# Kernel tuning notes

Measured on AMD Instinct MI355X. Metric: run time of the kernel, lower is better.

Reference implementation:

```python
import jax, jax.numpy as jnp
import numpy as np

T = 4096       # batch of observations
REPR = 2048    # repr_dim
FEAT = 1024    # feature_dim
HID = 1024     # hidden_dim (MoE input/output dim)
GATE = 256     # moe_gate_dim
MH = 256       # moe_hidden_dim (per-expert hidden)
E = 32         # num_experts
K = 4          # top_k
ACT = 12       # action dim
EPS = 1e-5


def setup_inputs() -> dict:
    key = jax.random.key(0)
    ks = jax.random.split(key, 18)

    def lin(k, fan_in, shape):
        return jax.random.normal(k, shape, jnp.float32) * (1.0 / np.sqrt(fan_in))

    return {
        "obs": jax.random.normal(ks[0], (T, REPR), jnp.float32),
        "std": jnp.ones((1,), jnp.float32),
        "trunk_w": lin(ks[1], REPR, (REPR, FEAT)),
        "trunk_b": jnp.zeros((FEAT,), jnp.float32),
        "ln_g": jnp.ones((FEAT,), jnp.float32),
        "ln_b": jnp.zeros((FEAT,), jnp.float32),
        "p1_w": lin(ks[2], FEAT, (FEAT, HID)),
        "p1_b": jnp.zeros((HID,), jnp.float32),
        "g1_w": lin(ks[3], HID, (HID, GATE)),
        "g1_b": jnp.zeros((GATE,), jnp.float32),
        "g2_w": lin(ks[4], GATE, (GATE, E)),
        "g2_b": jnp.zeros((E,), jnp.float32),
        "ew1": lin(ks[5], HID, (E, HID, MH)),
        "eb1": jnp.zeros((E, MH), jnp.float32),
        "ew2": lin(ks[6], MH, (E, MH, HID)),
        "eb2": jnp.zeros((E, HID), jnp.float32),
        "p2_w": lin(ks[7], HID, (HID, ACT)),
        "p2_b": jnp.zeros((ACT,), jnp.float32),
    }


def layer_norm(x, g, b):
    m = jnp.mean(x, -1, keepdims=True)
    v = jnp.var(x, -1, keepdims=True)
    return (x - m) * jax.lax.rsqrt(v + EPS) * g + b


def moe(x, g1_w, g1_b, g2_w, g2_b, ew1, eb1, ew2, eb2):
    # gate MLP: [T, HID] -> [T, E]
    logits = jax.nn.relu(x @ g1_w + g1_b) @ g2_w + g2_b
    probs = jax.nn.softmax(logits, axis=-1)                 # [T, E]
    topv, topi = jax.lax.top_k(probs, K)                    # [T, K]
    w = topv / jnp.sum(topv, -1, keepdims=True)             # renormalized top-k weights
    n = x.shape[0]
    combine = jnp.zeros((n, E), x.dtype).at[jnp.arange(n)[:, None], topi].set(w)  # [T, E]
    # per-expert 2-layer MLP (dense dispatch, masked combine)
    h = jax.nn.relu(jnp.einsum('td,edh->teh', x, ew1) + eb1)   # [T, E, MH]
    y = jnp.einsum('teh,eho->teo', h, ew2) + eb2               # [T, E, HID]
    out = jnp.einsum('te,teo->to', combine, y)                 # [T, HID]
    # load-balancing aux loss (switch-style)
    importance = jnp.mean(probs, axis=0)                                  # [E]
    load = jnp.sum(jax.nn.one_hot(topi, E, dtype=x.dtype), (0, 1)) / (n * K)
    aux = E * jnp.sum(importance * load)
    return out, aux


def reference(obs, std, trunk_w, trunk_b, ln_g, ln_b, p1_w, p1_b,
              g1_w, g1_b, g2_w, g2_b, ew1, eb1, ew2, eb2, p2_w, p2_b):
    h = jnp.tanh(layer_norm(obs @ trunk_w + trunk_b, ln_g, ln_b))
    x = jax.nn.relu(h @ p1_w + p1_b)
    x, aux = moe(x, g1_w, g1_b, g2_w, g2_b, ew1, eb1, ew2, eb2)
    mu = jnp.tanh(jax.nn.relu(x) @ p2_w + p2_b)
    std_out = jnp.ones_like(mu) * std
    return mu, std_out, aux
```

## Files before the change

kernel.cpp:

```cpp
#include <hip/hip_runtime.h>
#include <math.h>

#define T_DIM  4096
#define REPR_D 2048
#define FEAT_D 1024
#define HID_D  1024
#define GATE_D 256
#define MH_D   256
#define NE     32
#define TOPK   4
#define ACT_D  12
#define LN_EPS 1e-5f
#define NB_G   (T_DIM / 8)

typedef unsigned short u16;
typedef __attribute__((ext_vector_type(8))) _Float16 f16x8;
typedef __attribute__((ext_vector_type(4))) float f32x4;
typedef __attribute__((ext_vector_type(4))) unsigned short u16x4;

__device__ __forceinline__ u16 f2h_bits(float f) {
  _Float16 h = (_Float16)f;
  return __builtin_bit_cast(u16, h);
}
__device__ __forceinline__ float h2f(u16 v) {
  return (float)__builtin_bit_cast(_Float16, v);
}
__device__ __forceinline__ void split2h(float v, u16* h0, u16* h1) {
  _Float16 a = (_Float16)v;
  float r = v - (float)a;
  *h0 = __builtin_bit_cast(u16, a);
  *h1 = f2h_bits(r * 2048.0f);
}

__device__ __forceinline__ void gload16(const u16* g, u16* l) {
  __builtin_amdgcn_global_load_lds(
      (const __attribute__((address_space(1))) unsigned int*)g,
      (__attribute__((address_space(3))) unsigned int*)l, 16, 0, 0);
}

__global__ __launch_bounds__(256)
void gemm_f16x2_sk(const u16* __restrict__ A, const u16* __restrict__ Bt,
                   float* __restrict__ Cp, int M, int N, int K) {
  __shared__ u16 lA[2][128 * 64];
  __shared__ u16 lB[2][64 * 64];
  const int tid = threadIdx.x;
  const unsigned gx = gridDim.x, gy = gridDim.y;
  const unsigned lin = blockIdx.x + gx * (blockIdx.y + gy * blockIdx.z);
  const unsigned q = (gx * gy * gridDim.z) >> 3;
  const unsigned swz = (lin & 7) * q + (lin >> 3);
  const int bn = (swz % gx) * 64;
  const int bm = ((swz / gx) % gy) * 128;
  const int bz = swz / (gx * gy);
  const int ksl = K / gridDim.z;
  const int kbeg = bz * ksl, kend = kbeg + ksl;
  const int lane = tid & 63, wid = tid >> 6;
  const int wm = (wid >> 1) * 64, wn = (wid & 1) * 32;
  const size_t sA = (size_t)M * K, sB = (size_t)N * K;
  const int srow = tid >> 3;
  const int coff = ((tid & 7) ^ (srow & 7)) * 8;
  const u16* pa = A + (size_t)(bm + srow) * K + coff;
  const u16* pb = Bt + (size_t)(bn + srow) * K + coff;
  u16* la = &lA[0][0] + tid * 8;
  u16* lb = &lB[0][0] + tid * 8;
  const int fr = lane & 15, sx = lane >> 4, rx = lane & 7;
  f32x4 acc1[4][2] = {}, acc2[4][2] = {};
  for (int k0 = kbeg; k0 < kend; k0 += 64) {
    #pragma unroll
    for (int p = 0; p < 2; ++p) {
      #pragma unroll
      for (int s = 0; s < 4; ++s)
        gload16(pa + p * sA + (size_t)(s * 32) * K + k0, la + p * 8192 + s * 2048);
      #pragma unroll
      for (int s = 0; s < 2; ++s)
        gload16(pb + p * sB + (size_t)(s * 32) * K + k0, lb + p * 4096 + s * 2048);
    }
    __syncthreads();
    #pragma unroll
    for (int kh = 0; kh < 2; ++kh) {
      const int sa = (((kh << 2) | sx) ^ rx) * 8;
      f16x8 af0[4], af1[4], bq[2];
      #pragma unroll
      for (int m = 0; m < 4; ++m) {
        af0[m] = *(const f16x8*)&lA[0][(wm + m * 16 + fr) * 64 + sa];
        af1[m] = *(const f16x8*)&lA[1][(wm + m * 16 + fr) * 64 + sa];
      }
      #pragma unroll
      for (int n = 0; n < 2; ++n)
        bq[n] = *(const f16x8*)&lB[0][(wn + n * 16 + fr) * 64 + sa];
      #pragma unroll
      for (int m = 0; m < 4; ++m)
        #pragma unroll
        for (int n = 0; n < 2; ++n) {
          acc1[m][n] = __builtin_amdgcn_mfma_f32_16x16x32_f16(af0[m], bq[n], acc1[m][n], 0, 0, 0);
          acc2[m][n] = __builtin_amdgcn_mfma_f32_16x16x32_f16(af1[m], bq[n], acc2[m][n], 0, 0, 0);
        }
      #pragma unroll
      for (int n = 0; n < 2; ++n)
        bq[n] = *(const f16x8*)&lB[1][(wn + n * 16 + fr) * 64 + sa];
      #pragma unroll
      for (int m = 0; m < 4; ++m)
        #pragma unroll
        for (int n = 0; n < 2; ++n)
          acc2[m][n] = __builtin_amdgcn_mfma_f32_16x16x32_f16(af0[m], bq[n], acc2[m][n], 0, 0, 0);
    }
    __syncthreads();
  }
  float* Co = Cp + (size_t)bz * M * N;
  #pragma unroll
  for (int n = 0; n < 2; ++n) {
    const int col = bn + wn + n * 16 + (lane & 15);
    #pragma unroll
    for (int m = 0; m < 4; ++m) {
      #pragma unroll
      for (int r = 0; r < 4; ++r) {
        const int row = bm + wm + m * 16 + (lane >> 4) * 4 + r;
        Co[(size_t)row * N + col] = acc1[m][n][r] + acc2[m][n][r] * (1.0f / 2048.0f);
      }
    }
  }
}

__global__ __launch_bounds__(256)
void expert_l1(const u16* __restrict__ x, const u16* __restrict__ ew1T,
               const float* __restrict__ eb1, const int* __restrict__ perm,
               const int* __restrict__ offsets, const int* __restrict__ counts,
               u16* __restrict__ hbuf) {
  const int e = blockIdx.z;
  const int cnt = counts[e];
  const int r0 = blockIdx.y * 128;
  if (r0 >= cnt) return;
  const int base = offsets[e];
  const int bn = blockIdx.x * 64;
  __shared__ u16 lA[128 * 64];
  __shared__ u16 lB[64 * 64];
  __shared__ int toksm[128];
  const int tid = threadIdx.x;
  if (tid < 128) toksm[tid] = (r0 + tid < cnt) ? (perm[base + r0 + tid] >> 2) : 0;
  __syncthreads();
  const int lane = tid & 63, wid = tid >> 6;
  const int wm = (wid >> 1) * 64, wn = (wid & 1) * 32;
  const int srow = tid >> 3;
  const int coff = ((tid & 7) ^ (srow & 7)) * 8;
  const u16* pa[4]; const u16* pb[2];
  #pragma unroll
  for (int s = 0; s < 4; ++s)
    pa[s] = x + (size_t)toksm[srow + 32 * s] * HID_D + coff;
  #pragma unroll
  for (int s = 0; s < 2; ++s)
    pb[s] = ew1T + (size_t)e * MH_D * HID_D + (size_t)(bn + srow + 32 * s) * HID_D + coff;
  u16* la = lA + tid * 8;
  u16* lb = lB + tid * 8;
  const int fr = lane & 15, sx = lane >> 4, rx = lane & 7;
  f32x4 acc[4][2] = {};
  for (int k0 = 0; k0 < HID_D; k0 += 64) {
    #pragma unroll
    for (int s = 0; s < 4; ++s) gload16(pa[s] + k0, la + s * 2048);
    #pragma unroll
    for (int s = 0; s < 2; ++s) gload16(pb[s] + k0, lb + s * 2048);
    __syncthreads();
    #pragma unroll
    for (int kh = 0; kh < 2; ++kh) {
      const int sa = (((kh << 2) | sx) ^ rx) * 8;
      f16x8 af[4], bq[2];
      #pragma unroll
      for (int m = 0; m < 4; ++m)
        af[m] = *(const f16x8*)&lA[(wm + m * 16 + fr) * 64 + sa];
      #pragma unroll
      for (int n = 0; n < 2; ++n)
        bq[n] = *(const f16x8*)&lB[(wn + n * 16 + fr) * 64 + sa];
      #pragma unroll
      for (int m = 0; m < 4; ++m)
        #pragma unroll
        for (int n = 0; n < 2; ++n)
          acc[m][n] = __builtin_amdgcn_mfma_f32_16x16x32_f16(af[m], bq[n], acc[m][n], 0, 0, 0);
    }
    __syncthreads();
  }
  #pragma unroll
  for (int n = 0; n < 2; ++n) {
    const int col = bn + wn + n * 16 + (lane & 15);
    const float bz = eb1[e * MH_D + col];
    #pragma unroll
    for (int m = 0; m < 4; ++m) {
      #pragma unroll
      for (int r = 0; r < 4; ++r) {
        const int rl = wm + m * 16 + (lane >> 4) * 4 + r;
        if (r0 + rl < cnt) {
          const float v = fmaxf(acc[m][n][r] + bz, 0.f);
          hbuf[(size_t)(base + r0 + rl) * MH_D + col] = f2h_bits(v);
        }
      }
    }
  }
}

__global__ __launch_bounds__(256)
void expert_l2(const u16* __restrict__ hbuf, const u16* __restrict__ ew2T,
               const float* __restrict__ eb2, const int* __restrict__ offsets,
               const int* __restrict__ counts, u16* __restrict__ ybuf) {
  const int e = blockIdx.z;
  const int cnt = counts[e];
  const int r0 = blockIdx.y * 128;
  if (r0 >= cnt) return;
  const int base = offsets[e];
  const int bn = blockIdx.x * 64;
  __shared__ u16 lA[128 * 64];
  __shared__ u16 lB[64 * 64];
  const int tid = threadIdx.x;
  const int lane = tid & 63, wid = tid >> 6;
  const int wm = (wid >> 1) * 64, wn = (wid & 1) * 32;
  const int srow = tid >> 3;
  const int coff = ((tid & 7) ^ (srow & 7)) * 8;
  const u16* pa[4]; const u16* pb[2];
  #pragma unroll
  for (int s = 0; s < 4; ++s) {
    const int rr = r0 + srow + 32 * s;
    const int rc = (rr < cnt) ? rr : cnt - 1;
    pa[s] = hbuf + (size_t)(base + rc) * MH_D + coff;
  }
  #pragma unroll
  for (int s = 0; s < 2; ++s)
    pb[s] = ew2T + (size_t)e * HID_D * MH_D + (size_t)(bn + srow + 32 * s) * MH_D + coff;
  u16* la = lA + tid * 8;
  u16* lb = lB + tid * 8;
  const int fr = lane & 15, sx = lane >> 4, rx = lane & 7;
  f32x4 acc[4][2] = {};
  for (int k0 = 0; k0 < MH_D; k0 += 64) {
    #pragma unroll
    for (int s = 0; s < 4; ++s) gload16(pa[s] + k0, la + s * 2048);
    #pragma unroll
    for (int s = 0; s < 2; ++s) gload16(pb[s] + k0, lb + s * 2048);
    __syncthreads();
    #pragma unroll
    for (int kh = 0; kh < 2; ++kh) {
      const int sa = (((kh << 2) | sx) ^ rx) * 8;
      f16x8 af[4], bq[2];
      #pragma unroll
      for (int m = 0; m < 4; ++m)
        af[m] = *(const f16x8*)&lA[(wm + m * 16 + fr) * 64 + sa];
      #pragma unroll
      for (int n = 0; n < 2; ++n)
        bq[n] = *(const f16x8*)&lB[(wn + n * 16 + fr) * 64 + sa];
      #pragma unroll
      for (int m = 0; m < 4; ++m)
        #pragma unroll
        for (int n = 0; n < 2; ++n)
          acc[m][n] = __builtin_amdgcn_mfma_f32_16x16x32_f16(af[m], bq[n], acc[m][n], 0, 0, 0);
    }
    __syncthreads();
  }
  #pragma unroll
  for (int n = 0; n < 2; ++n) {
    const int col = bn + wn + n * 16 + (lane & 15);
    const float bz = eb2[e * HID_D + col];
    #pragma unroll
    for (int m = 0; m < 4; ++m) {
      #pragma unroll
      for (int r = 0; r < 4; ++r) {
        const int rl = wm + m * 16 + (lane >> 4) * 4 + r;
        if (r0 + rl < cnt)
          ybuf[(size_t)(base + r0 + rl) * HID_D + col] = f2h_bits(acc[m][n][r] + bz);
      }
    }
  }
}

__global__ __launch_bounds__(256)
void cast2h_k(const float* __restrict__ in, u16* __restrict__ out, size_t total) {
  const size_t i = ((size_t)blockIdx.x * 256 + threadIdx.x) * 4;
  const float4 v = *(const float4*)(in + i);
  const float vv[4] = {v.x, v.y, v.z, v.w};
  u16x4 o0, o1;
  #pragma unroll
  for (int j = 0; j < 4; ++j) {
    u16 a, b;
    split2h(vv[j], &a, &b);
    o0[j] = a; o1[j] = b;
  }
  *(u16x4*)(out + i) = o0;
  *(u16x4*)(out + total + i) = o1;
}

__global__ __launch_bounds__(256)
void transpose_cast2h(const float* __restrict__ in, u16* __restrict__ out, int K, int N) {
  __shared__ float t[32][33];
  const int bn = blockIdx.x * 32, bk = blockIdx.y * 32;
  const int tx = threadIdx.x & 31, ty = threadIdx.x >> 5;
  const size_t NK = (size_t)N * K;
  #pragma unroll
  for (int i = 0; i < 32; i += 8) t[ty + i][tx] = in[(size_t)(bk + ty + i) * N + bn + tx];
  __syncthreads();
  #pragma unroll
  for (int i = 0; i < 32; i += 8) {
    const size_t idx = (size_t)(bn + ty + i) * K + bk + tx;
    u16 h0, h1;
    split2h(t[tx][ty + i], &h0, &h1);
    out[idx] = h0; out[idx + NK] = h1;
  }
}

__global__ __launch_bounds__(256)
void transpose_casth(const float* __restrict__ in, u16* __restrict__ out, int K, int N) {
  const size_t off = (size_t)blockIdx.z * K * N;
  in += off; out += off;
  __shared__ float t[32][33];
  const int bn = blockIdx.x * 32, bk = blockIdx.y * 32;
  const int tx = threadIdx.x & 31, ty = threadIdx.x >> 5;
  #pragma unroll
  for (int i = 0; i < 32; i += 8) t[ty + i][tx] = in[(size_t)(bk + ty + i) * N + bn + tx];
  __syncthreads();
  #pragma unroll
  for (int i = 0; i < 32; i += 8) out[(size_t)(bn + ty + i) * K + bk + tx] = f2h_bits(t[tx][ty + i]);
}

__global__ __launch_bounds__(256)
void ln_tanh2h(const float* __restrict__ hp, const float* __restrict__ tb,
               u16* __restrict__ outp, const float* __restrict__ g,
               const float* __restrict__ b) {
  const int row = blockIdx.x, tid = threadIdx.x;
  const size_t MN = (size_t)T_DIM * FEAT_D;
  const float4 va = ((const float4*)(hp + (size_t)row * FEAT_D))[tid];
  const float4 vb = ((const float4*)(hp + MN + (size_t)row * FEAT_D))[tid];
  const float4 vt = ((const float4*)tb)[tid];
  float4 v;
  v.x = va.x + vb.x + vt.x; v.y = va.y + vb.y + vt.y;
  v.z = va.z + vb.z + vt.z; v.w = va.w + vb.w + vt.w;
  float s = v.x + v.y + v.z + v.w;
  float ss = v.x * v.x + v.y * v.y + v.z * v.z + v.w * v.w;
  #pragma unroll
  for (int d = 32; d >= 1; d >>= 1) { s += __shfl_xor(s, d, 64); ss += __shfl_xor(ss, d, 64); }
  __shared__ float red[2][4];
  const int w = tid >> 6;
  if ((tid & 63) == 0) { red[0][w] = s; red[1][w] = ss; }
  __syncthreads();
  s  = red[0][0] + red[0][1] + red[0][2] + red[0][3];
  ss = red[1][0] + red[1][1] + red[1][2] + red[1][3];
  const float m = s * (1.f / FEAT_D);
  const float inv = rsqrtf(ss * (1.f / FEAT_D) - m * m + LN_EPS);
  const float4 gg = ((const float4*)g)[tid];
  const float4 bb = ((const float4*)b)[tid];
  const float tv[4] = {tanhf((v.x - m) * inv * gg.x + bb.x),
                       tanhf((v.y - m) * inv * gg.y + bb.y),
                       tanhf((v.z - m) * inv * gg.z + bb.z),
                       tanhf((v.w - m) * inv * gg.w + bb.w)};
  u16x4 o0, o1;
  #pragma unroll
  for (int j = 0; j < 4; ++j) {
    u16 a, c;
    split2h(tv[j], &a, &c);
    o0[j] = a; o1[j] = c;
  }
  ((u16x4*)(outp + (size_t)row * FEAT_D))[tid] = o0;
  ((u16x4*)(outp + MN + (size_t)row * FEAT_D))[tid] = o1;
}

__global__ __launch_bounds__(256)
void combine2_relu_split2h(const float* __restrict__ P, const float* __restrict__ bias,
                           u16* __restrict__ out2) {
  const size_t MN = (size_t)T_DIM * HID_D;
  const size_t i = ((size_t)blockIdx.x * 256 + threadIdx.x) * 4;
  const float4 a = *(const float4*)(P + i);
  const float4 b = *(const float4*)(P + MN + i);
  const float4 bz = *(const float4*)(bias + (i & (HID_D - 1)));
  const float vv[4] = {fmaxf(a.x + b.x + bz.x, 0.f), fmaxf(a.y + b.y + bz.y, 0.f),
                       fmaxf(a.z + b.z + bz.z, 0.f), fmaxf(a.w + b.w + bz.w, 0.f)};
  u16x4 o0, o1;
  #pragma unroll
  for (int j = 0; j < 4; ++j) {
    u16 h0, h1;
    split2h(vv[j], &h0, &h1);
    o0[j] = h0; o1[j] = h1;
  }
  *(u16x4*)(out2 + i) = o0;
  *(u16x4*)(out2 + MN + i) = o1;
}

__global__ __launch_bounds__(256)
void gate2_topk(const float* __restrict__ hgP, const float* __restrict__ g1b,
                const float* __restrict__ g2w, const float* __restrict__ g2b,
                float* __restrict__ blkimp, int* __restrict__ blkcnt,
                int* __restrict__ topi, float* __restrict__ topw,
                int* __restrict__ lrank) {
  __shared__ float wsm[GATE_D][NE];
  __shared__ float rows[8][GATE_D];
  __shared__ float pacc[8][NE];
  __shared__ int lhist[NE];
  const int tid = threadIdx.x;
  const int t0 = blockIdx.x * 8;
  const size_t TG = (size_t)T_DIM * GATE_D;
  if (tid < NE) lhist[tid] = 0;
  {
    float4* wv = (float4*)&wsm[0][0];
    const float4* gv = (const float4*)g2w;
    #pragma unroll
    for (int i = 0; i < 8; ++i) wv[tid + 256 * i] = gv[tid + 256 * i];
  }
  {
    const float4* p0 = (const float4*)hgP;
    const float4* p1 = (const float4*)(hgP + TG);
    const float4* p2 = (const float4*)(hgP + 2 * TG);
    const float4* p3 = (const float4*)(hgP + 3 * TG);
    const float4* bv = (const float4*)g1b;
    float4* rv = (float4*)&rows[0][0];
    #pragma unroll
    for (int i = 0; i < 2; ++i) {
      const int idx = tid + 256 * i;
      const int r = idx >> 6, c4 = idx & 63;
      const size_t gidx = (size_t)(t0 + r) * (GATE_D / 4) + c4;
      const float4 a = p0[gidx], b = p1[gidx], c = p2[gidx], d = p3[gidx];
      const float4 bb = bv[c4];
      float4 v;
      v.x = fmaxf(a.x + b.x + c.x + d.x + bb.x, 0.f);
      v.y = fmaxf(a.y + b.y + c.y + d.y + bb.y, 0.f);
      v.z = fmaxf(a.z + b.z + c.z + d.z + bb.z, 0.f);
      v.w = fmaxf(a.w + b.w + c.w + d.w + bb.w, 0.f);
      rv[idx] = v;
    }
  }
  __syncthreads();
  const int tl = tid >> 5;
  const int e  = tid & 31;
  const int t  = t0 + tl;
  float a8[8] = {};
  #pragma unroll
  for (int k0 = 0; k0 < GATE_D; k0 += 8)
    #pragma unroll
    for (int j = 0; j < 8; ++j)
      a8[j] = fmaf(rows[tl][k0 + j], wsm[k0 + j][e], a8[j]);
  const float logit = g2b[e] +
      (((a8[0] + a8[1]) + (a8[2] + a8[3])) + ((a8[4] + a8[5]) + (a8[6] + a8[7])));
  float m = logit;
  #pragma unroll
  for (int d = 16; d >= 1; d >>= 1) m = fmaxf(m, __shfl_xor(m, d, 32));
  const float p = expf(logit - m);
  float ssum = p;
  #pragma unroll
  for (int d = 16; d >= 1; d >>= 1) ssum += __shfl_xor(ssum, d, 32);
  const float prob = p / ssum;
  pacc[tl][e] = prob;
  __syncthreads();
  if (tl == 0) {
    float a = 0.f;
    #pragma unroll
    for (int q = 0; q < 8; ++q) a += pacc[q][e];
    blkimp[blockIdx.x * NE + e] = a;
  }
  float cur = prob;
  float wv[TOPK]; int wi[TOPK];
  #pragma unroll
  for (int it = 0; it < TOPK; ++it) {
    float v = cur; int idx = e;
    #pragma unroll
    for (int d = 16; d >= 1; d >>= 1) {
      float v2 = __shfl_xor(v, d, 32);
      int   i2 = __shfl_xor(idx, d, 32);
      if (v2 > v || (v2 == v && i2 < idx)) { v = v2; idx = i2; }
    }
    wv[it] = v; wi[it] = idx;
    if (e == idx) cur = -1e30f;
  }
  if (e == 0) {
    const float s4 = wv[0] + wv[1] + wv[2] + wv[3];
    #pragma unroll
    for (int k2 = 0; k2 < TOPK; ++k2) {
      topi[t * TOPK + k2] = wi[k2];
      topw[t * TOPK + k2] = wv[k2] / s4;
      lrank[t * TOPK + k2] = atomicAdd(&lhist[wi[k2]], 1);
    }
  }
  __syncthreads();
  if (tid < NE) blkcnt[blockIdx.x * NE + tid] = lhist[tid];
}

__global__ __launch_bounds__(256)
void scan_k(const int* __restrict__ blkcnt, int* __restrict__ counts,
            int* __restrict__ offsets, int* __restrict__ blkbase) {
  __shared__ int segsum[8][NE];
  __shared__ int soff[8][NE];
  const int e = threadIdx.x & 31, seg = threadIdx.x >> 5;
  const int b0 = seg * 64;
  int vals[64];
  #pragma unroll
  for (int i = 0; i < 64; ++i) vals[i] = blkcnt[(b0 + i) * NE + e];
  int run = 0;
  #pragma unroll
  for (int i = 0; i < 64; ++i) { const int c = vals[i]; vals[i] = run; run += c; }
  segsum[seg][e] = run;
  __syncthreads();
  if (seg == 0) {
    int acc = 0;
    #pragma unroll
    for (int s2 = 0; s2 < 8; ++s2) { soff[s2][e] = acc; acc += segsum[s2][e]; }
    counts[e] = acc;
  }
  __syncthreads();
  if (threadIdx.x == 0) {
    int a = 0;
    for (int i = 0; i < NE; ++i) { offsets[i] = a; a += counts[i]; }
    offsets[NE] = a;
  }
  const int sb = soff[seg][e];
  #pragma unroll
  for (int i = 0; i < 64; ++i) blkbase[(b0 + i) * NE + e] = sb + vals[i];
}

__global__ __launch_bounds__(256)
void fill_perm2(const int* __restrict__ topi, const int* __restrict__ lrank,
                const int* __restrict__ blkbase, const int* __restrict__ offsets,
                int* __restrict__ perm, int* __restrict__ inv) {
  const int s = blockIdx.x * 256 + threadIdx.x;
  const int e = topi[s];
  const int b = s >> 5;
  const int pos = offsets[e] + blkbase[b * NE + e] + lrank[s];
  perm[pos] = s;
  inv[s] = pos;
}

__global__ __launch_bounds__(256)
void p2_head(const u16* __restrict__ ybuf, const int* __restrict__ inv,
             const float* __restrict__ topw, const float* __restrict__ w,
             const float* __restrict__ b, const float* __restrict__ stdp,
             float* __restrict__ outp) {
  const int t = (blockIdx.x * 256 + threadIdx.x) >> 6;
  const int lane = threadIdx.x & 63;
  if (t >= T_DIM) return;
  const int p0 = inv[t * 4 + 0], p1 = inv[t * 4 + 1];
  const int p2 = inv[t * 4 + 2], p3 = inv[t * 4 + 3];
  const float w0 = topw[t * 4 + 0], w1 = topw[t * 4 + 1];
  const float w2 = topw[t * 4 + 2], w3 = topw[t * 4 + 3];
  const u16* y0 = ybuf + (size_t)p0 * HID_D;
  const u16* y1 = ybuf + (size_t)p1 * HID_D;
  const u16* y2 = ybuf + (size_t)p2 * HID_D;
  const u16* y3 = ybuf + (size_t)p3 * HID_D;
  float a[ACT_D] = {};
  for (int k = lane; k < HID_D; k += 64) {
    float xv = w0 * h2f(y0[k]) + w1 * h2f(y1[k]) + w2 * h2f(y2[k]) + w3 * h2f(y3[k]);
    xv = fmaxf(xv, 0.f);
    const float* wr = w + (size_t)k * ACT_D;
    #pragma unroll
    for (int j = 0; j < ACT_D; ++j) a[j] = fmaf(xv, wr[j], a[j]);
  }
  #pragma unroll
  for (int j = 0; j < ACT_D; ++j) {
    float v = a[j];
    #pragma unroll
    for (int d = 32; d >= 1; d >>= 1) v += __shfl_xor(v, d, 64);
    a[j] = v;
  }
  if (lane == 0) {
    const float sv = stdp[0];
    #pragma unroll
    for (int j = 0; j < ACT_D; ++j) {
      outp[(size_t)t * ACT_D + j] = tanhf(a[j] + b[j]);
      outp[(size_t)T_DIM * ACT_D + (size_t)t * ACT_D + j] = sv;
    }
  }
}

__global__ __launch_bounds__(256)
void aux_kernel(const float* __restrict__ blkimp, const int* __restrict__ counts,
                float* __restrict__ outp) {
  __shared__ float part[8][NE];
  const int e = threadIdx.x & 31, seg = threadIdx.x >> 5;
  float a = 0.f;
  #pragma unroll
  for (int i = 0; i < 64; ++i) a += blkimp[((seg << 6) + i) * NE + e];
  part[seg][e] = a;
  __syncthreads();
  if (threadIdx.x < 32) {
    float impe = 0.f;
    #pragma unroll
    for (int s2 = 0; s2 < 8; ++s2) impe += part[s2][e];
    float v = (impe / (float)T_DIM) * ((float)counts[e] / (float)(T_DIM * TOPK));
    #pragma unroll
    for (int d = 16; d >= 1; d >>= 1) v += __shfl_xor(v, d, 32);
    if (e == 0) outp[2 * T_DIM * ACT_D] = (float)NE * v;
  }
}

extern "C" void kernel_launch(void* const* d_in, const int* in_sizes, int n_in,
                              void* d_out, int out_size, void* d_ws, size_t ws_size,
                              hipStream_t stream) {
  const float* obs     = (const float*)d_in[0];
  const float* stdp    = (const float*)d_in[1];
  const float* trunk_w = (const float*)d_in[2];
  const float* trunk_b = (const float*)d_in[3];
  const float* ln_g    = (const float*)d_in[4];
  const float* ln_b    = (const float*)d_in[5];
  const float* p1_w    = (const float*)d_in[6];
  const float* p1_b    = (const float*)d_in[7];
  const float* g1_w    = (const float*)d_in[8];
  const float* g1_b    = (const float*)d_in[9];
  const float* g2_w    = (const float*)d_in[10];
  const float* g2_b    = (const float*)d_in[11];
  const float* ew1     = (const float*)d_in[12];
  const float* eb1     = (const float*)d_in[13];
  const float* ew2     = (const float*)d_in[14];
  const float* eb2     = (const float*)d_in[15];
  const float* p2_w    = (const float*)d_in[16];
  const float* p2_b    = (const float*)d_in[17];
  float* out = (float*)d_out;

  char* p = (char*)d_ws;
  u16*   obs2 = (u16*)p;
  u16*   h2   = (u16*)p;
  float* hgP  = (float*)p;
  u16*   x2   = (u16*)(p + 2 * (size_t)T_DIM * FEAT_D * 2);
  p += 2 * (size_t)T_DIM * REPR_D * 2;
  u16* trunk_wT2 = (u16*)p;
  u16* p1_wT2    = (u16*)p;
  u16* g1_wT2    = (u16*)(p + 2 * (size_t)FEAT_D * HID_D * 2);
  u16* hbuf      = (u16*)p;
  p += 2 * (size_t)REPR_D * FEAT_D * 2;
  float* hpP  = (float*)p;
  float* p1P  = (float*)p;
  u16*   ybuf = (u16*)p;
  p += 2 * (size_t)T_DIM * FEAT_D * 4;
  u16* ew1T = (u16*)p; p += (size_t)NE * HID_D * MH_D * 2;
  u16* ew2T = (u16*)p; p += (size_t)NE * HID_D * MH_D * 2;
  float* topw    = (float*)p; p += (size_t)T_DIM * TOPK * 4;
  int*   topi    = (int*)p;   p += (size_t)T_DIM * TOPK * 4;
  int*   perm    = (int*)p;   p += (size_t)T_DIM * TOPK * 4;
  int*   inv     = (int*)p;   p += (size_t)T_DIM * TOPK * 4;
  int*   lrank   = (int*)p;   p += (size_t)T_DIM * TOPK * 4;
  float* blkimp  = (float*)p; p += (size_t)NB_G * NE * 4;
  int*   blkcnt  = (int*)p;   p += (size_t)NB_G * NE * 4;
  int*   blkbase = (int*)p;   p += (size_t)NB_G * NE * 4;
  int*   counts  = (int*)p;   p += 128;
  int*   offsets = (int*)p;   p += 256;

  cast2h_k<<<(T_DIM * REPR_D) / 1024, 256, 0, stream>>>(obs, obs2, (size_t)T_DIM * REPR_D);
  transpose_cast2h<<<dim3(FEAT_D / 32, REPR_D / 32), 256, 0, stream>>>(trunk_w, trunk_wT2, REPR_D, FEAT_D);

  gemm_f16x2_sk<<<dim3(FEAT_D / 64, T_DIM / 128, 2), 256, 0, stream>>>(
      obs2, trunk_wT2, hpP, T_DIM, FEAT_D, REPR_D);
  transpose_cast2h<<<dim3(HID_D / 32, FEAT_D / 32), 256, 0, stream>>>(p1_w, p1_wT2, FEAT_D, HID_D);
  transpose_cast2h<<<dim3(GATE_D / 32, HID_D / 32), 256, 0, stream>>>(g1_w, g1_wT2, HID_D, GATE_D);

  ln_tanh2h<<<T_DIM, 256, 0, stream>>>(hpP, trunk_b, h2, ln_g, ln_b);

  gemm_f16x2_sk<<<dim3(HID_D / 64, T_DIM / 128, 2), 256, 0, stream>>>(
      h2, p1_wT2, p1P, T_DIM, HID_D, FEAT_D);
  combine2_relu_split2h<<<(T_DIM * HID_D) / 1024, 256, 0, stream>>>(p1P, p1_b, x2);

  gemm_f16x2_sk<<<dim3(GATE_D / 64, T_DIM / 128, 4), 256, 0, stream>>>(
      x2, g1_wT2, hgP, T_DIM, GATE_D, HID_D);

  gate2_topk<<<NB_G, 256, 0, stream>>>(hgP, g1_b, g2_w, g2_b, blkimp, blkcnt, topi, topw, lrank);
  scan_k<<<1, 256, 0, stream>>>(blkcnt, counts, offsets, blkbase);
  fill_perm2<<<(T_DIM * TOPK) / 256, 256, 0, stream>>>(topi, lrank, blkbase, offsets, perm, inv);

  transpose_casth<<<dim3(MH_D / 32, HID_D / 32, NE), 256, 0, stream>>>(ew1, ew1T, HID_D, MH_D);
  transpose_casth<<<dim3(HID_D / 32, MH_D / 32, NE), 256, 0, stream>>>(ew2, ew2T, MH_D, HID_D);
  expert_l1<<<dim3(MH_D / 64, 32, NE), 256, 0, stream>>>(
      x2, ew1T, eb1, perm, offsets, counts, hbuf);
  expert_l2<<<dim3(HID_D / 64, 32, NE), 256, 0, stream>>>(
      hbuf, ew2T, eb2, offsets, counts, ybuf);

  p2_head<<<T_DIM / 4, 256, 0, stream>>>(ybuf, inv, topw, p2_w, p2_b, stdp, out);
  aux_kernel<<<1, 256, 0, stream>>>(blkimp, counts, out);
}
```

Before: 268.4 us.

## Double-buffer LDS in GEMM and expert kernels with 32-wide K stages; vectorize head loads

The split-K GEMM and both expert MLP kernels now stage K in 32-element slices into two LDS buffers. The next slice's global-to-LDS load is issued while MFMAs run on the current one, which takes one barrier per stage off the critical load path, and the XOR swizzle is reworked to match the narrower rows. The p2 head also reads expert outputs with 4-wide vector loads instead of scalar half loads. The trade is more barriers overall from halving the K step, and less latency hiding if the loads do not complete behind the compute.

New measurement: 298.1 us. +11.1%, slower.

```diff
diff --git a/kernel.cpp b/kernel.cpp
--- a/kernel.cpp
+++ b/kernel.cpp
@@ -41,8 +41,8 @@
 __global__ __launch_bounds__(256)
 void gemm_f16x2_sk(const u16* __restrict__ A, const u16* __restrict__ Bt,
                    float* __restrict__ Cp, int M, int N, int K) {
-  __shared__ u16 lA[2][128 * 64];
-  __shared__ u16 lB[2][64 * 64];
+  __shared__ u16 lA[2 * 2 * 128 * 32];
+  __shared__ u16 lB[2 * 2 * 64 * 32];
   const int tid = threadIdx.x;
   const unsigned gx = gridDim.x, gy = gridDim.y;
   const unsigned lin = blockIdx.x + gx * (blockIdx.y + gy * blockIdx.z);
@@ -52,57 +52,65 @@
   const int bm = ((swz / gx) % gy) * 128;
   const int bz = swz / (gx * gy);
   const int ksl = K / gridDim.z;
-  const int kbeg = bz * ksl, kend = kbeg + ksl;
+  const int kbeg = bz * ksl;
+  const int nst = ksl / 32;
   const int lane = tid & 63, wid = tid >> 6;
   const int wm = (wid >> 1) * 64, wn = (wid & 1) * 32;
   const size_t sA = (size_t)M * K, sB = (size_t)N * K;
-  const int srow = tid >> 3;
-  const int coff = ((tid & 7) ^ (srow & 7)) * 8;
-  const u16* pa = A + (size_t)(bm + srow) * K + coff;
-  const u16* pb = Bt + (size_t)(bn + srow) * K + coff;
-  u16* la = &lA[0][0] + tid * 8;
-  u16* lb = &lB[0][0] + tid * 8;
-  const int fr = lane & 15, sx = lane >> 4, rx = lane & 7;
+  const u16* pa[4]; const u16* pb[2];
+  #pragma unroll
+  for (int s = 0; s < 4; ++s) {
+    const int c = tid + 256 * s;
+    const int pl = c >> 9, r = (c >> 2) & 127, sl = c & 3;
+    pa[s] = A + (size_t)pl * sA + (size_t)(bm + r) * K + kbeg + ((sl ^ ((r >> 1) & 3)) << 3);
+  }
+  #pragma unroll
+  for (int s = 0; s < 2; ++s) {
+    const int c = tid + 256 * s;
+    const int pl = c >> 8, r = (c >> 2) & 63, sl = c & 3;
+    pb[s] = Bt + (size_t)pl * sB + (size_t)(bn + r) * K + kbeg + ((sl ^ ((r >> 1) & 3)) << 3);
+  }
+  const int fr = lane & 15, sx = lane >> 4;
   f32x4 acc1[4][2] = {}, acc2[4][2] = {};
-  for (int k0 = kbeg; k0 < kend; k0 += 64) {
-    #pragma unroll
-    for (int p = 0; p < 2; ++p) {
-      #pragma unroll
-      for (int s = 0; s < 4; ++s)
-        gload16(pa + p * sA + (size_t)(s * 32) * K + k0, la + p * 8192 + s * 2048);
-      #pragma unroll
-      for (int s = 0; s < 2; ++s)
-        gload16(pb + p * sB + (size_t)(s * 32) * K + k0, lb + p * 4096 + s * 2048);
-    }
-    __syncthreads();
-    #pragma unroll
-    for (int kh = 0; kh < 2; ++kh) {
-      const int sa = (((kh << 2) | sx) ^ rx) * 8;
-      f16x8 af0[4], af1[4], bq[2];
-      #pragma unroll
-      for (int m = 0; m < 4; ++m) {
-        af0[m] = *(const f16x8*)&lA[0][(wm + m * 16 + fr) * 64 + sa];
-        af1[m] = *(const f16x8*)&lA[1][(wm + m * 16 + fr) * 64 + sa];
+  #pragma unroll
+  for (int s = 0; s < 4; ++s) gload16(pa[s], lA + (tid + 256 * s) * 8);
+  #pragma unroll
+  for (int s = 0; s < 2; ++s) gload16(pb[s], lB + (tid + 256 * s) * 8);
+  __syncthreads();
+  for (int t = 0; t < nst; ++t) {
+    const int cur = t & 1, nxt = cur ^ 1;
+    if (t + 1 < nst) {
+      const int kk = (t + 1) * 32;
+      #pragma unroll
+      for (int s = 0; s < 4; ++s) gload16(pa[s] + kk, lA + nxt * 8192 + (tid + 256 * s) * 8);
+      #pragma unroll
+      for (int s = 0; s < 2; ++s) gload16(pb[s] + kk, lB + nxt * 4096 + (tid + 256 * s) * 8);
+    }
+    const u16* bufA = lA + cur * 8192;
+    const u16* bufB = lB + cur * 4096;
+    f16x8 af0[4], af1[4], bq0[2], bq1[2];
+    #pragma unroll
+    for (int m = 0; m < 4; ++m) {
+      const int row = wm + m * 16 + fr;
+      const int so = (sx ^ ((row >> 1) & 3)) << 3;
+      af0[m] = *(const f16x8*)&bufA[row * 32 + so];
+      af1[m] = *(const f16x8*)&bufA[4096 + row * 32 + so];
+    }
+    #pragma unroll
+    for (int n = 0; n < 2; ++n) {
+      const int row = wn + n * 16 + fr;
+      const int so = (sx ^ ((row >> 1) & 3)) << 3;
+      bq0[n] = *(const f16x8*)&bufB[row * 32 + so];
+      bq1[n] = *(const f16x8*)&bufB[2048 + row * 32 + so];
+    }
+    #pragma unroll
+    for (int m = 0; m < 4; ++m)
+      #pragma unroll
+      for (int n = 0; n < 2; ++n) {
+        acc1[m][n] = __builtin_amdgcn_mfma_f32_16x16x32_f16(af0[m], bq0[n], acc1[m][n], 0, 0, 0);
+        acc2[m][n] = __builtin_amdgcn_mfma_f32_16x16x32_f16(af1[m], bq0[n], acc2[m][n], 0, 0, 0);
+        acc2[m][n] = __builtin_amdgcn_mfma_f32_16x16x32_f16(af0[m], bq1[n], acc2[m][n], 0, 0, 0);
       }
-      #pragma unroll
-      for (int n = 0; n < 2; ++n)
-        bq[n] = *(const f16x8*)&lB[0][(wn + n * 16 + fr) * 64 + sa];
-      #pragma unroll
-      for (int m = 0; m < 4; ++m)
-        #pragma unroll
-        for (int n = 0; n < 2; ++n) {
-          acc1[m][n] = __builtin_amdgcn_mfma_f32_16x16x32_f16(af0[m], bq[n], acc1[m][n], 0, 0, 0);
-          acc2[m][n] = __builtin_amdgcn_mfma_f32_16x16x32_f16(af1[m], bq[n], acc2[m][n], 0, 0, 0);
-        }
-      #pragma unroll
-      for (int n = 0; n < 2; ++n)
-        bq[n] = *(const f16x8*)&lB[1][(wn + n * 16 + fr) * 64 + sa];
-      #pragma unroll
-      for (int m = 0; m < 4; ++m)
-        #pragma unroll
-        for (int n = 0; n < 2; ++n)
-          acc2[m][n] = __builtin_amdgcn_mfma_f32_16x16x32_f16(af0[m], bq[n], acc2[m][n], 0, 0, 0);
-    }
     __syncthreads();
   }
   float* Co = Cp + (size_t)bz * M * N;
@@ -131,49 +139,58 @@
   if (r0 >= cnt) return;
   const int base = offsets[e];
   const int bn = blockIdx.x * 64;
-  __shared__ u16 lA[128 * 64];
-  __shared__ u16 lB[64 * 64];
+  __shared__ u16 lA[2 * 128 * 32];
+  __shared__ u16 lB[2 * 64 * 32];
   __shared__ int toksm[128];
   const int tid = threadIdx.x;
   if (tid < 128) toksm[tid] = (r0 + tid < cnt) ? (perm[base + r0 + tid] >> 2) : 0;
   __syncthreads();
   const int lane = tid & 63, wid = tid >> 6;
   const int wm = (wid >> 1) * 64, wn = (wid & 1) * 32;
-  const int srow = tid >> 3;
-  const int coff = ((tid & 7) ^ (srow & 7)) * 8;
-  const u16* pa[4]; const u16* pb[2];
-  #pragma unroll
-  for (int s = 0; s < 4; ++s)
-    pa[s] = x + (size_t)toksm[srow + 32 * s] * HID_D + coff;
-  #pragma unroll
-  for (int s = 0; s < 2; ++s)
-    pb[s] = ew1T + (size_t)e * MH_D * HID_D + (size_t)(bn + srow + 32 * s) * HID_D + coff;
-  u16* la = lA + tid * 8;
-  u16* lb = lB + tid * 8;
-  const int fr = lane & 15, sx = lane >> 4, rx = lane & 7;
+  const u16* pa[2]; const u16* pb;
+  #pragma unroll
+  for (int s = 0; s < 2; ++s) {
+    const int c = tid + 256 * s;
+    const int r = c >> 2, sl = c & 3;
+    pa[s] = x + (size_t)toksm[r] * HID_D + ((sl ^ ((r >> 1) & 3)) << 3);
+  }
+  {
+    const int r = tid >> 2, sl = tid & 3;
+    pb = ew1T + (size_t)e * MH_D * HID_D + (size_t)(bn + r) * HID_D + ((sl ^ ((r >> 1) & 3)) << 3);
+  }
+  const int fr = lane & 15, sx = lane >> 4;
   f32x4 acc[4][2] = {};
-  for (int k0 = 0; k0 < HID_D; k0 += 64) {
-    #pragma unroll
-    for (int s = 0; s < 4; ++s) gload16(pa[s] + k0, la + s * 2048);
-    #pragma unroll
-    for (int s = 0; s < 2; ++s) gload16(pb[s] + k0, lb + s * 2048);
-    __syncthreads();
-    #pragma unroll
-    for (int kh = 0; kh < 2; ++kh) {
-      const int sa = (((kh << 2) | sx) ^ rx) * 8;
-      f16x8 af[4], bq[2];
-      #pragma unroll
-      for (int m = 0; m < 4; ++m)
-        af[m] = *(const f16x8*)&lA[(wm + m * 16 + fr) * 64 + sa];
+  #pragma unroll
+  for (int s = 0; s < 2; ++s) gload16(pa[s], lA + (tid + 256 * s) * 8);
+  gload16(pb, lB + tid * 8);
+  __syncthreads();
+  const int nst = HID_D / 32;
+  for (int t = 0; t < nst; ++t) {
+    const int cur = t & 1, nxt = cur ^ 1;
+    if (t + 1 < nst) {
+      const int kk = (t + 1) * 32;
+      #pragma unroll
+      for (int s = 0; s < 2; ++s) gload16(pa[s] + kk, lA + nxt * 4096 + (tid + 256 * s) * 8);
+      gload16(pb + kk, lB + nxt * 2048 + tid * 8);
+    }
+    const u16* bufA = lA + cur * 4096;
+    const u16* bufB = lB + cur * 2048;
+    f16x8 af[4], bq[2];
+    #pragma unroll
+    for (int m = 0; m < 4; ++m) {
+      const int row = wm + m * 16 + fr;
+      af[m] = *(const f16x8*)&bufA[row * 32 + ((sx ^ ((row >> 1) & 3)) << 3)];
+    }
+    #pragma unroll
+    for (int n = 0; n < 2; ++n) {
+      const int row = wn + n * 16 + fr;
+      bq[n] = *(const f16x8*)&bufB[row * 32 + ((sx ^ ((row >> 1) & 3)) << 3)];
+    }
+    #pragma unroll
+    for (int m = 0; m < 4; ++m)
       #pragma unroll
       for (int n = 0; n < 2; ++n)
-        bq[n] = *(const f16x8*)&lB[(wn + n * 16 + fr) * 64 + sa];
-      #pragma unroll
-      for (int m = 0; m < 4; ++m)
-        #pragma unroll
-        for (int n = 0; n < 2; ++n)
-          acc[m][n] = __builtin_amdgcn_mfma_f32_16x16x32_f16(af[m], bq[n], acc[m][n], 0, 0, 0);
-    }
+        acc[m][n] = __builtin_amdgcn_mfma_f32_16x16x32_f16(af[m], bq[n], acc[m][n], 0, 0, 0);
     __syncthreads();
   }
   #pragma unroll
@@ -204,49 +221,57 @@
   if (r0 >= cnt) return;
   const int base = offsets[e];
   const int bn = blockIdx.x * 64;
-  __shared__ u16 lA[128 * 64];
-  __shared__ u16 lB[64 * 64];
+  __shared__ u16 lA[2 * 128 * 32];
+  __shared__ u16 lB[2 * 64 * 32];
   const int tid = threadIdx.x;
   const int lane = tid & 63, wid = tid >> 6;
   const int wm = (wid >> 1) * 64, wn = (wid & 1) * 32;
-  const int srow = tid >> 3;
-  const int coff = ((tid & 7) ^ (srow & 7)) * 8;
-  const u16* pa[4]; const u16* pb[2];
-  #pragma unroll
-  for (int s = 0; s < 4; ++s) {
-    const int rr = r0 + srow + 32 * s;
+  const u16* pa[2]; const u16* pb;
+  #pragma unroll
+  for (int s = 0; s < 2; ++s) {
+    const int c = tid + 256 * s;
+    const int r = c >> 2, sl = c & 3;
+    const int rr = r0 + r;
     const int rc = (rr < cnt) ? rr : cnt - 1;
-    pa[s] = hbuf + (size_t)(base + rc) * MH_D + coff;
-  }
-  #pragma unroll
-  for (int s = 0; s < 2; ++s)
-    pb[s] = ew2T + (size_t)e * HID_D * MH_D + (size_t)(bn + srow + 32 * s) * MH_D + coff;
-  u16* la = lA + tid * 8;
-  u16* lb = lB + tid * 8;
-  const int fr = lane & 15, sx = lane >> 4, rx = lane & 7;
+    pa[s] = hbuf + (size_t)(base + rc) * MH_D + ((sl ^ ((r >> 1) & 3)) << 3);
+  }
+  {
+    const int r = tid >> 2, sl = tid & 3;
+    pb = ew2T + (size_t)e * HID_D * MH_D + (size_t)(bn + r) * MH_D + ((sl ^ ((r >> 1) & 3)) << 3);
+  }
+  const int fr = lane & 15, sx = lane >> 4;
   f32x4 acc[4][2] = {};
-  for (int k0 = 0; k0 < MH_D; k0 += 64) {
-    #pragma unroll
-    for (int s = 0; s < 4; ++s) gload16(pa[s] + k0, la + s * 2048);
-    #pragma unroll
-    for (int s = 0; s < 2; ++s) gload16(pb[s] + k0, lb + s * 2048);
-    __syncthreads();
-    #pragma unroll
-    for (int kh = 0; kh < 2; ++kh) {
-      const int sa = (((kh << 2) | sx) ^ rx) * 8;
-      f16x8 af[4], bq[2];
-      #pragma unroll
-      for (int m = 0; m < 4; ++m)
-        af[m] = *(const f16x8*)&lA[(wm + m * 16 + fr) * 64 + sa];
+  #pragma unroll
+  for (int s = 0; s < 2; ++s) gload16(pa[s], lA + (tid + 256 * s) * 8);
+  gload16(pb, lB + tid * 8);
+  __syncthreads();
+  const int nst = MH_D / 32;
+  for (int t = 0; t < nst; ++t) {
+    const int cur = t & 1, nxt = cur ^ 1;
+    if (t + 1 < nst) {
+      const int kk = (t + 1) * 32;
+      #pragma unroll
+      for (int s = 0; s < 2; ++s) gload16(pa[s] + kk, lA + nxt * 4096 + (tid + 256 * s) * 8);
+      gload16(pb + kk, lB + nxt * 2048 + tid * 8);
+    }
+    const u16* bufA = lA + cur * 4096;
+    const u16* bufB = lB + cur * 2048;
+    f16x8 af[4], bq[2];
+    #pragma unroll
+    for (int m = 0; m < 4; ++m) {
+      const int row = wm + m * 16 + fr;
+      af[m] = *(const f16x8*)&bufA[row * 32 + ((sx ^ ((row >> 1) & 3)) << 3)];
+    }
+    #pragma unroll
+    for (int n = 0; n < 2; ++n) {
+      const int row = wn + n * 16 + fr;
+      bq[n] = *(const f16x8*)&bufB[row * 32 + ((sx ^ ((row >> 1) & 3)) << 3)];
+    }
+    #pragma unroll
+    for (int m = 0; m < 4; ++m)
       #pragma unroll
       for (int n = 0; n < 2; ++n)
-        bq[n] = *(const f16x8*)&lB[(wn + n * 16 + fr) * 64 + sa];
-      #pragma unroll
-      for (int m = 0; m < 4; ++m)
-        #pragma unroll
-        for (int n = 0; n < 2; ++n)
-          acc[m][n] = __builtin_amdgcn_mfma_f32_16x16x32_f16(af[m], bq[n], acc[m][n], 0, 0, 0);
-    }
+        acc[m][n] = __builtin_amdgcn_mfma_f32_16x16x32_f16(af[m], bq[n], acc[m][n], 0, 0, 0);
     __syncthreads();
   }
   #pragma unroll
@@ -533,12 +558,21 @@
   const u16* y2 = ybuf + (size_t)p2 * HID_D;
   const u16* y3 = ybuf + (size_t)p3 * HID_D;
   float a[ACT_D] = {};
-  for (int k = lane; k < HID_D; k += 64) {
-    float xv = w0 * h2f(y0[k]) + w1 * h2f(y1[k]) + w2 * h2f(y2[k]) + w3 * h2f(y3[k]);
-    xv = fmaxf(xv, 0.f);
-    const float* wr = w + (size_t)k * ACT_D;
-    #pragma unroll
-    for (int j = 0; j < ACT_D; ++j) a[j] = fmaf(xv, wr[j], a[j]);
+  #pragma unroll
+  for (int k0 = 0; k0 < 4; ++k0) {
+    const int kb = k0 * 256 + lane * 4;
+    const u16x4 va = *(const u16x4*)(y0 + kb);
+    const u16x4 vb = *(const u16x4*)(y1 + kb);
+    const u16x4 vc = *(const u16x4*)(y2 + kb);
+    const u16x4 vd = *(const u16x4*)(y3 + kb);
+    #pragma unroll
+    for (int j = 0; j < 4; ++j) {
+      float xv = w0 * h2f(va[j]) + w1 * h2f(vb[j]) + w2 * h2f(vc[j]) + w3 * h2f(vd[j]);
+      xv = fmaxf(xv, 0.f);
+      const float* wr = w + (size_t)(kb + j) * ACT_D;
+      #pragma unroll
+      for (int jj = 0; jj < ACT_D; ++jj) a[jj] = fmaf(xv, wr[jj], a[jj]);
+    }
   }
   #pragma unroll
   for (int j = 0; j < ACT_D; ++j) {
```

## Double-buffer split-K f16x2 GEMM with async LDS prefetch and vectorize head loads

Applied to the files above, without the earlier changes.

The split-K GEMM moves from a single 64-wide K stage with two full syncthreads per iteration to 32-wide K stages held in two LDS buffers. The load for stage t+2 is issued while stage t computes, using explicit vmcnt waits and raw s_barrier calls, so global-to-LDS latency overlaps the MFMA work. The LDS swizzle is changed to match the 32-column rows. Separately, the p2 head now reads the four gathered expert rows as 4-wide u16 vectors instead of scalar halves. Risks are the hand-written waitcnt counts, which must match the number of outstanding loads, and the shorter K step, which adds barrier overhead per unit of work.

Result: slower. 291.4 us (+8.6%).

```diff
diff --git a/kernel.cpp b/kernel.cpp
--- a/kernel.cpp
+++ b/kernel.cpp
@@ -38,11 +38,27 @@
       (__attribute__((address_space(3))) unsigned int*)l, 16, 0, 0);
 }
 
+__device__ __forceinline__ void sbar() {
+  __builtin_amdgcn_sched_barrier(0);
+  asm volatile("" ::: "memory");
+  __builtin_amdgcn_s_barrier();
+  asm volatile("" ::: "memory");
+  __builtin_amdgcn_sched_barrier(0);
+}
+__device__ __forceinline__ void vwait6() {
+  asm volatile("s_waitcnt vmcnt(6)" ::: "memory");
+  __builtin_amdgcn_sched_barrier(0);
+}
+__device__ __forceinline__ void vwait0() {
+  asm volatile("s_waitcnt vmcnt(0)" ::: "memory");
+  __builtin_amdgcn_sched_barrier(0);
+}
+
 __global__ __launch_bounds__(256)
 void gemm_f16x2_sk(const u16* __restrict__ A, const u16* __restrict__ Bt,
                    float* __restrict__ Cp, int M, int N, int K) {
-  __shared__ u16 lA[2][128 * 64];
-  __shared__ u16 lB[2][64 * 64];
+  __shared__ u16 lA[2 * 2 * 128 * 32];
+  __shared__ u16 lB[2 * 2 * 64 * 32];
   const int tid = threadIdx.x;
   const unsigned gx = gridDim.x, gy = gridDim.y;
   const unsigned lin = blockIdx.x + gx * (blockIdx.y + gy * blockIdx.z);
@@ -52,58 +68,73 @@
   const int bm = ((swz / gx) % gy) * 128;
   const int bz = swz / (gx * gy);
   const int ksl = K / gridDim.z;
-  const int kbeg = bz * ksl, kend = kbeg + ksl;
+  const int kbeg = bz * ksl;
+  const int nst = ksl / 32;
   const int lane = tid & 63, wid = tid >> 6;
   const int wm = (wid >> 1) * 64, wn = (wid & 1) * 32;
   const size_t sA = (size_t)M * K, sB = (size_t)N * K;
-  const int srow = tid >> 3;
-  const int coff = ((tid & 7) ^ (srow & 7)) * 8;
-  const u16* pa = A + (size_t)(bm + srow) * K + coff;
-  const u16* pb = Bt + (size_t)(bn + srow) * K + coff;
-  u16* la = &lA[0][0] + tid * 8;
-  u16* lb = &lB[0][0] + tid * 8;
-  const int fr = lane & 15, sx = lane >> 4, rx = lane & 7;
+  const u16* pa[4]; const u16* pb[2];
+  #pragma unroll
+  for (int s = 0; s < 4; ++s) {
+    const int c = tid + 256 * s;
+    const int pl = c >> 9, r = (c >> 2) & 127, sl = c & 3;
+    pa[s] = A + (size_t)pl * sA + (size_t)(bm + r) * K + kbeg + ((sl ^ ((r >> 1) & 3)) << 3);
+  }
+  #pragma unroll
+  for (int s = 0; s < 2; ++s) {
+    const int c = tid + 256 * s;
+    const int pl = c >> 8, r = (c >> 2) & 63, sl = c & 3;
+    pb[s] = Bt + (size_t)pl * sB + (size_t)(bn + r) * K + kbeg + ((sl ^ ((r >> 1) & 3)) << 3);
+  }
+  const int fr = lane & 15, sx = lane >> 4;
   f32x4 acc1[4][2] = {}, acc2[4][2] = {};
-  for (int k0 = kbeg; k0 < kend; k0 += 64) {
-    #pragma unroll
-    for (int p = 0; p < 2; ++p) {
-      #pragma unroll
-      for (int s = 0; s < 4; ++s)
-        gload16(pa + p * sA + (size_t)(s * 32) * K + k0, la + p * 8192 + s * 2048);
-      #pragma unroll
-      for (int s = 0; s < 2; ++s)
-        gload16(pb + p * sB + (size_t)(s * 32) * K + k0, lb + p * 4096 + s * 2048);
-    }
-    __syncthreads();
-    #pragma unroll
-    for (int kh = 0; kh < 2; ++kh) {
-      const int sa = (((kh << 2) | sx) ^ rx) * 8;
-      f16x8 af0[4], af1[4], bq[2];
-      #pragma unroll
-      for (int m = 0; m < 4; ++m) {
-        af0[m] = *(const f16x8*)&lA[0][(wm + m * 16 + fr) * 64 + sa];
-        af1[m] = *(const f16x8*)&lA[1][(wm + m * 16 + fr) * 64 + sa];
+  #pragma unroll
+  for (int s = 0; s < 4; ++s) gload16(pa[s], lA + (tid + 256 * s) * 8);
+  #pragma unroll
+  for (int s = 0; s < 2; ++s) gload16(pb[s], lB + (tid + 256 * s) * 8);
+  if (nst > 1) {
+    #pragma unroll
+    for (int s = 0; s < 4; ++s) gload16(pa[s] + 32, lA + 8192 + (tid + 256 * s) * 8);
+    #pragma unroll
+    for (int s = 0; s < 2; ++s) gload16(pb[s] + 32, lB + 4096 + (tid + 256 * s) * 8);
+  }
+  for (int t = 0; t < nst; ++t) {
+    const int cur = t & 1;
+    if (t + 1 < nst) vwait6(); else vwait0();
+    sbar();
+    const u16* bufA = lA + cur * 8192;
+    const u16* bufB = lB + cur * 4096;
+    f16x8 af0[4], af1[4], bq0[2], bq1[2];
+    #pragma unroll
+    for (int m = 0; m < 4; ++m) {
+      const int row = wm + m * 16 + fr;
+      const int so = (sx ^ ((row >> 1) & 3)) << 3;
+      af0[m] = *(const f16x8*)&bufA[row * 32 + so];
+      af1[m] = *(const f16x8*)&bufA[4096 + row * 32 + so];
+    }
+    #pragma unroll
+    for (int n = 0; n < 2; ++n) {
+      const int row = wn + n * 16 + fr;
+      const int so = (sx ^ ((row >> 1) & 3)) << 3;
+      bq0[n] = *(const f16x8*)&bufB[row * 32 + so];
+      bq1[n] = *(const f16x8*)&bufB[2048 + row * 32 + so];
+    }
+    #pragma unroll
+    for (int m = 0; m < 4; ++m)
+      #pragma unroll
+      for (int n = 0; n < 2; ++n) {
+        acc1[m][n] = __builtin_amdgcn_mfma_f32_16x16x32_f16(af0[m], bq0[n], acc1[m][n], 0, 0, 0);
+        acc2[m][n] = __builtin_amdgcn_mfma_f32_16x16x32_f16(af1[m], bq0[n], acc2[m][n], 0, 0, 0);
+        acc2[m][n] = __builtin_amdgcn_mfma_f32_16x16x32_f16(af0[m], bq1[n], acc2[m][n], 0, 0, 0);
       }
-      #pragma unroll
-      for (int n = 0; n < 2; ++n)
-        bq[n] = *(const f16x8*)&lB[0][(wn + n * 16 + fr) * 64 + sa];
-      #pragma unroll
-      for (int m = 0; m < 4; ++m)
-        #pragma unroll
-        for (int n = 0; n < 2; ++n) {
-          acc1[m][n] = __builtin_amdgcn_mfma_f32_16x16x32_f16(af0[m], bq[n], acc1[m][n], 0, 0, 0);
-          acc2[m][n] = __builtin_amdgcn_mfma_f32_16x16x32_f16(af1[m], bq[n], acc2[m][n], 0, 0, 0);
-        }
-      #pragma unroll
-      for (int n = 0; n < 2; ++n)
-        bq[n] = *(const f16x8*)&lB[1][(wn + n * 16 + fr) * 64 + sa];
-      #pragma unroll
-      for (int m = 0; m < 4; ++m)
-        #pragma unroll
-        for (int n = 0; n < 2; ++n)
-          acc2[m][n] = __builtin_amdgcn_mfma_f32_16x16x32_f16(af0[m], bq[n], acc2[m][n], 0, 0, 0);
-    }
-    __syncthreads();
+    sbar();
+    if (t + 2 < nst) {
+      const int kk = (t + 2) * 32;
+      #pragma unroll
+      for (int s = 0; s < 4; ++s) gload16(pa[s] + kk, lA + cur * 8192 + (tid + 256 * s) * 8);
+      #pragma unroll
+      for (int s = 0; s < 2; ++s) gload16(pb[s] + kk, lB + cur * 4096 + (tid + 256 * s) * 8);
+    }
   }
   float* Co = Cp + (size_t)bz * M * N;
   #pragma unroll
@@ -533,12 +564,21 @@
   const u16* y2 = ybuf + (size_t)p2 * HID_D;
   const u16* y3 = ybuf + (size_t)p3 * HID_D;
   float a[ACT_D] = {};
-  for (int k = lane; k < HID_D; k += 64) {
-    float xv = w0 * h2f(y0[k]) + w1 * h2f(y1[k]) + w2 * h2f(y2[k]) + w3 * h2f(y3[k]);
-    xv = fmaxf(xv, 0.f);
-    const float* wr = w + (size_t)k * ACT_D;
-    #pragma unroll
-    for (int j = 0; j < ACT_D; ++j) a[j] = fmaf(xv, wr[j], a[j]);
+  #pragma unroll
+  for (int k0 = 0; k0 < 4; ++k0) {
+    const int kb = k0 * 256 + lane * 4;
+    const u16x4 va = *(const u16x4*)(y0 + kb);
+    const u16x4 vb = *(const u16x4*)(y1 + kb);
+    const u16x4 vc = *(const u16x4*)(y2 + kb);
+    const u16x4 vd = *(const u16x4*)(y3 + kb);
+    #pragma unroll
+    for (int j = 0; j < 4; ++j) {
+      float xv = w0 * h2f(va[j]) + w1 * h2f(vb[j]) + w2 * h2f(vc[j]) + w3 * h2f(vd[j]);
+      xv = fmaxf(xv, 0.f);
+      const float* wr = w + (size_t)(kb + j) * ACT_D;
+      #pragma unroll
+      for (int jj = 0; jj < ACT_D; ++jj) a[jj] = fmaf(xv, wr[jj], a[jj]);
+    }
   }
   #pragma unroll
   for (int j = 0; j < ACT_D; ++j) {
```
